# Kernel tuning notes

Measured on AMD Instinct MI355X. Metric: run time of the kernel, lower is better.

## Reference

```python
import jax, jax.numpy as jnp
import numpy as np

B, S, D = 2, 2048, 2048
H, DH = 16, 128
F = 5504
EPS = 1e-6
ROPE_THETA = 10000.0


def setup_inputs() -> dict:
    key = jax.random.key(0)
    ks = jax.random.split(key, 20)
    sc = 0.02
    r = lambda k, shape: (jax.random.normal(k, shape, dtype=jnp.float32) * sc)
    return {
        "hidden_states": jax.random.normal(ks[0], (B, S, D), dtype=jnp.float32),
        "ln1_w": jnp.ones((D,), jnp.float32),
        "wq": r(ks[1], (H * DH, D)), "bq": jnp.zeros((H * DH,), jnp.float32),
        "wk": r(ks[2], (H * DH, D)), "bk": jnp.zeros((H * DH,), jnp.float32),
        "wv": r(ks[3], (H * DH, D)), "bv": jnp.zeros((H * DH,), jnp.float32),
        "wo": r(ks[4], (D, H * DH)),
        "ln2_w": jnp.ones((D,), jnp.float32),
        "e1_gate": r(ks[5], (F, D)), "e1_up": r(ks[6], (F, D)), "e1_down": r(ks[7], (D, F)),
        "e2_gate": r(ks[8], (F, D)), "e2_up": r(ks[9], (F, D)), "e2_down": r(ks[10], (D, F)),
        "router_w": r(ks[11], (2, D)), "router_b": jnp.zeros((2,), jnp.float32),
    }


def rmsnorm(x, w):
    v = jnp.mean(x.astype(jnp.float32) ** 2, axis=-1, keepdims=True)
    return (x * jax.lax.rsqrt(v + EPS)).astype(x.dtype) * w


def rotate_half(x):
    x1, x2 = jnp.split(x, 2, axis=-1)
    return jnp.concatenate([-x2, x1], axis=-1)


def rope_cos_sin(seq_len, dtype):
    inv = 1.0 / (ROPE_THETA ** (jnp.arange(0, DH, 2, dtype=jnp.float32) / DH))
    t = jnp.arange(seq_len, dtype=jnp.float32)
    freqs = jnp.outer(t, inv)                      # [S, DH/2]
    emb = jnp.concatenate([freqs, freqs], axis=-1)  # [S, DH]
    return jnp.cos(emb).astype(dtype), jnp.sin(emb).astype(dtype)


def mlp(x, gate, up, down):
    return jnp.einsum('bsf,df->bsd', jax.nn.silu(jnp.einsum('bsd,fd->bsf', x, gate))
                      * jnp.einsum('bsd,fd->bsf', x, up), down)


def reference(hidden_states, ln1_w, wq, bq, wk, bk, wv, bv, wo, ln2_w,
              e1_gate, e1_up, e1_down, e2_gate, e2_up, e2_down,
              router_w, router_b):
    residual = hidden_states
    h = rmsnorm(hidden_states, ln1_w)

    # --- self attention with RoPE, causal ---
    q = (h @ wq.T + bq).reshape(B, S, H, DH).transpose(0, 2, 1, 3)  # [B,H,S,DH]
    k = (h @ wk.T + bk).reshape(B, S, H, DH).transpose(0, 2, 1, 3)
    v = (h @ wv.T + bv).reshape(B, S, H, DH).transpose(0, 2, 1, 3)
    cos, sin = rope_cos_sin(S, q.dtype)
    q = q * cos + rotate_half(q) * sin
    k = k * cos + rotate_half(k) * sin
    scores = jnp.einsum('bhqd,bhkd->bhqk', q, k) / jnp.sqrt(jnp.float32(DH))
    causal = jnp.tril(jnp.ones((S, S), dtype=bool))
    scores = jnp.where(causal, scores, jnp.finfo(scores.dtype).min)
    attn = jax.nn.softmax(scores, axis=-1)
    ctx = jnp.einsum('bhqk,bhkd->bhqd', attn, v).transpose(0, 2, 1, 3).reshape(B, S, H * DH)
    h = residual + ctx @ wo.T

    # --- MoE block: top-1 over 2 experts, both computed densely (as in source) ---
    residual = h
    h = rmsnorm(h, ln2_w)
    router_logits = h @ router_w.T + router_b          # [B,S,2]
    router_probs = jax.nn.softmax(router_logits, axis=-1)
    choice = jnp.argmax(router_probs, axis=-1)          # [B,S]
    m1 = (choice == 0).astype(h.dtype)[..., None]
    m2 = (choice == 1).astype(h.dtype)[..., None]
    out1 = mlp(h, e1_gate, e1_up, e1_down)
    out2 = mlp(h, e2_gate, e2_up, e2_down)
    return residual + m1 * out1 + m2 * out2
```

## Files before the change

kernel.cpp:

```cpp
#include <hip/hip_runtime.h>
#include <math.h>

typedef unsigned short u16;
typedef unsigned int u32;

#define D_ 2048
#define S_ 2048
#define DH_ 128
#define NH_ 16
#define F_ 5504
#define MTOK 4096

typedef __bf16 bf16x8 __attribute__((ext_vector_type(8)));
typedef float f32x4 __attribute__((ext_vector_type(4)));

__device__ __forceinline__ float bf2f(u32 u) {
  union { u32 i; float f; } x; x.i = u << 16; return x.f;
}
__device__ __forceinline__ u16 f2bf(float f) {
  u32 x = __float_as_uint(f);
  return (u16)((x + 0x7fffu + ((x >> 16) & 1u)) >> 16);
}

__global__ __launch_bounds__(256)
void k_f2bf(const float* __restrict__ src, u16* __restrict__ dst) {
  const size_t i = ((size_t)blockIdx.x * 256 + threadIdx.x) * 8;
  float4 a = *(const float4*)(src + i);
  float4 b = *(const float4*)(src + i + 4);
  uint4 p;
  p.x = f2bf(a.x) | ((u32)f2bf(a.y) << 16);
  p.y = f2bf(a.z) | ((u32)f2bf(a.w) << 16);
  p.z = f2bf(b.x) | ((u32)f2bf(b.y) << 16);
  p.w = f2bf(b.z) | ((u32)f2bf(b.w) << 16);
  *(uint4*)(dst + i) = p;
}

__global__ __launch_bounds__(256)
void k_moe_init(int* __restrict__ cnt, int* __restrict__ idx) {
  const int tid = threadIdx.x;
  if (tid < 2) cnt[tid] = 0;
  for (int i = tid; i < 2 * MTOK; i += 256) idx[i] = 0;
}

__global__ __launch_bounds__(256)
void k_rmsnorm1(const float* __restrict__ x, const float* __restrict__ w,
                u16* __restrict__ out) {
  const int t = blockIdx.x, tid = threadIdx.x;
  const size_t off = (size_t)t * D_ + tid * 8;
  float4 x0 = *(const float4*)(x + off);
  float4 x1 = *(const float4*)(x + off + 4);
  float v[8] = {x0.x, x0.y, x0.z, x0.w, x1.x, x1.y, x1.z, x1.w};
  float ss = 0.f;
  #pragma unroll
  for (int i = 0; i < 8; ++i) ss += v[i] * v[i];
  #pragma unroll
  for (int o = 32; o > 0; o >>= 1) ss += __shfl_xor(ss, o, 64);
  __shared__ float red[4];
  if ((tid & 63) == 0) red[tid >> 6] = ss;
  __syncthreads();
  const float tot = red[0] + red[1] + red[2] + red[3];
  const float rstd = 1.0f / sqrtf(tot / (float)D_ + 1e-6f);
  float4 w0 = *(const float4*)(w + tid * 8);
  float4 w1 = *(const float4*)(w + tid * 8 + 4);
  float wv[8] = {w0.x, w0.y, w0.z, w0.w, w1.x, w1.y, w1.z, w1.w};
  u32 hb[8];
  #pragma unroll
  for (int i = 0; i < 8; ++i) hb[i] = f2bf(v[i] * rstd * wv[i]);
  uint4 up;
  up.x = hb[0] | (hb[1] << 16); up.y = hb[2] | (hb[3] << 16);
  up.z = hb[4] | (hb[5] << 16); up.w = hb[6] | (hb[7] << 16);
  *(uint4*)(out + off) = up;
}

__global__ __launch_bounds__(256)
void k_rmsnorm2_router(const float* __restrict__ xin, const float* __restrict__ w,
                       const float* __restrict__ rw, const float* __restrict__ rb,
                       u16* __restrict__ h2, int* __restrict__ cnt,
                       int* __restrict__ idx) {
  const int t = blockIdx.x, tid = threadIdx.x;
  const size_t off = (size_t)t * D_ + tid * 8;
  float4 x0 = *(const float4*)(xin + off);
  float4 x1 = *(const float4*)(xin + off + 4);
  float v[8] = {x0.x, x0.y, x0.z, x0.w, x1.x, x1.y, x1.z, x1.w};
  float ss = 0.f;
  #pragma unroll
  for (int i = 0; i < 8; ++i) ss += v[i] * v[i];
  #pragma unroll
  for (int o = 32; o > 0; o >>= 1) ss += __shfl_xor(ss, o, 64);
  __shared__ float red[4];
  __shared__ float rl[8];
  if ((tid & 63) == 0) red[tid >> 6] = ss;
  __syncthreads();
  const float tot = red[0] + red[1] + red[2] + red[3];
  const float rstd = 1.0f / sqrtf(tot / (float)D_ + 1e-6f);
  float4 w0 = *(const float4*)(w + tid * 8);
  float4 w1 = *(const float4*)(w + tid * 8 + 4);
  float wv[8] = {w0.x, w0.y, w0.z, w0.w, w1.x, w1.y, w1.z, w1.w};
  float4 ra = *(const float4*)(rw + tid * 8);
  float4 rb4 = *(const float4*)(rw + tid * 8 + 4);
  float4 rc = *(const float4*)(rw + D_ + tid * 8);
  float4 rd = *(const float4*)(rw + D_ + tid * 8 + 4);
  float r0[8] = {ra.x, ra.y, ra.z, ra.w, rb4.x, rb4.y, rb4.z, rb4.w};
  float r1[8] = {rc.x, rc.y, rc.z, rc.w, rd.x, rd.y, rd.z, rd.w};
  float l0 = 0.f, l1 = 0.f;
  u32 hb[8];
  #pragma unroll
  for (int i = 0; i < 8; ++i) {
    const float h = v[i] * rstd * wv[i];
    hb[i] = f2bf(h);
    l0 += h * r0[i];
    l1 += h * r1[i];
  }
  uint4 up;
  up.x = hb[0] | (hb[1] << 16); up.y = hb[2] | (hb[3] << 16);
  up.z = hb[4] | (hb[5] << 16); up.w = hb[6] | (hb[7] << 16);
  *(uint4*)(h2 + off) = up;
  #pragma unroll
  for (int o = 32; o > 0; o >>= 1) {
    l0 += __shfl_xor(l0, o, 64);
    l1 += __shfl_xor(l1, o, 64);
  }
  if ((tid & 63) == 0) { rl[tid >> 6] = l0; rl[4 + (tid >> 6)] = l1; }
  __syncthreads();
  if (tid == 0) {
    const float L0 = rl[0] + rl[1] + rl[2] + rl[3] + rb[0];
    const float L1 = rl[4] + rl[5] + rl[6] + rl[7] + rb[1];
    const int e = (L1 > L0) ? 1 : 0;
    const int slot = atomicAdd(&cnt[e], 1);
    idx[e * MTOK + slot] = t;
  }
}

__global__ __launch_bounds__(256)
void k_rope_bf(const float* __restrict__ Q, const float* __restrict__ K,
               u16* __restrict__ Qo, u16* __restrict__ Ko) {
  const int t = blockIdx.x;
  const int s = t & (S_ - 1);
  const int d = threadIdx.x & 63;
  const int hq = threadIdx.x >> 6;
  const double inv = pow(10000.0, -(double)d / 64.0);
  const double ang = (double)s * inv;
  const float cf = (float)cos(ang);
  const float sf = (float)sin(ang);
  const float sc = 0.088388347648318447f;
  #pragma unroll
  for (int i = 0; i < 4; ++i) {
    const int h = hq * 4 + i;
    const size_t idx = (size_t)t * D_ + h * DH_ + d;
    float x1 = Q[idx], x2 = Q[idx + 64];
    Qo[idx]      = f2bf((x1 * cf - x2 * sf) * sc);
    Qo[idx + 64] = f2bf((x2 * cf + x1 * sf) * sc);
    float y1 = K[idx], y2 = K[idx + 64];
    Ko[idx]      = f2bf(y1 * cf - y2 * sf);
    Ko[idx + 64] = f2bf(y2 * cf + y1 * sf);
  }
}

__global__ __launch_bounds__(256)
void k_attn_mfma(const u16* __restrict__ Qbf, const u16* __restrict__ Kbf,
                 const u16* __restrict__ Vbf, u16* __restrict__ O) {
  __shared__ u16 Ks[64 * 128];
  __shared__ u16 Vt[128 * 64];
  __shared__ u16 Ps[4 * 16 * 64];
  const int qx = blockIdx.x, h = blockIdx.y, b = blockIdx.z;
  const int qt = (qx & 1) ? (31 - (qx >> 1)) : (qx >> 1);
  const int tid = threadIdx.x;
  const int w = tid >> 6, lane = tid & 63;
  const int quad = lane >> 4, l16 = lane & 15;

  const int q0 = qt * 64 + w * 16;
  const size_t qrow = (size_t)(b * S_ + q0 + l16) * D_ + h * DH_;
  bf16x8 qf[4];
  #pragma unroll
  for (int kd = 0; kd < 4; ++kd)
    qf[kd] = *(const bf16x8*)(Qbf + qrow + kd * 32 + quad * 8);

  f32x4 acc_o[8];
  #pragma unroll
  for (int i = 0; i < 8; ++i) acc_o[i] = 0;
  float mrun[4], lrun[4];
  #pragma unroll
  for (int r = 0; r < 4; ++r) { mrun[r] = -INFINITY; lrun[r] = 0.f; }

  const int nkt = qt + 1;
  const int vk = tid >> 2;
  const int vd0 = (tid & 3) * 32;

  for (int jt = 0; jt < nkt; ++jt) {
    const int kv0 = jt * 64;
    #pragma unroll
    for (int i = 0; i < 4; ++i) {
      const int slot = w * 256 + i * 64 + lane;
      const int r = slot >> 4, c = slot & 15;
      const int clog = (c & 8) | ((c & 7) ^ (r & 7));
      __builtin_amdgcn_global_load_lds(
        (const __attribute__((address_space(1))) void*)
          (Kbf + (size_t)(b * S_ + kv0 + r) * D_ + h * DH_ + clog * 8),
        (__attribute__((address_space(3))) void*)(Ks + (w * 256 + i * 64) * 8),
        16, 0, 0);
    }
    #pragma unroll
    for (int rr = 0; rr < 4; ++rr) {
      const int d0 = vd0 + rr * 8;
      bf16x8 vv = *(const bf16x8*)(Vbf + (size_t)(b * S_ + kv0 + vk) * D_ + h * DH_ + d0);
      const u16* pv = (const u16*)&vv;
      #pragma unroll
      for (int e = 0; e < 8; ++e) {
        const int d = d0 + e;
        Vt[d * 64 + ((((vk >> 3) ^ (d & 7) ^ ((d >> 5) & 3)) & 7) << 3) + (vk & 7)] = pv[e];
      }
    }
    __syncthreads();

    f32x4 st[4];
    #pragma unroll
    for (int nt = 0; nt < 4; ++nt) st[nt] = 0;
    #pragma unroll
    for (int kd = 0; kd < 4; ++kd) {
      #pragma unroll
      for (int nt = 0; nt < 4; ++nt) {
        const int kvr = nt * 16 + l16;
        const int c = kd * 4 + quad;
        const int p = (c & 8) | ((c & 7) ^ (kvr & 7));
        bf16x8 kf = *(const bf16x8*)(Ks + kvr * 128 + p * 8);
        st[nt] = __builtin_amdgcn_mfma_f32_16x16x32_bf16(qf[kd], kf, st[nt], 0, 0, 0);
      }
    }
    if (jt == qt) {
      #pragma unroll
      for (int nt = 0; nt < 4; ++nt) {
        const int kv = kv0 + nt * 16 + l16;
        #pragma unroll
        for (int r = 0; r < 4; ++r) {
          const int q = qt * 64 + w * 16 + quad * 4 + r;
          if (kv > q) st[nt][r] = -INFINITY;
        }
      }
    }
    float mx[4];
    #pragma unroll
    for (int r = 0; r < 4; ++r)
      mx[r] = fmaxf(fmaxf(st[0][r], st[1][r]), fmaxf(st[2][r], st[3][r]));
    #pragma unroll
    for (int o = 1; o < 16; o <<= 1) {
      #pragma unroll
      for (int r = 0; r < 4; ++r) mx[r] = fmaxf(mx[r], __shfl_xor(mx[r], o, 64));
    }
    float alpha[4], psum[4];
    #pragma unroll
    for (int r = 0; r < 4; ++r) {
      const float mnew = fmaxf(mrun[r], mx[r]);
      alpha[r] = expf(mrun[r] - mnew);
      mrun[r] = mnew;
      psum[r] = 0.f;
    }
    u16 pb[4][4];
    #pragma unroll
    for (int nt = 0; nt < 4; ++nt) {
      #pragma unroll
      for (int r = 0; r < 4; ++r) {
        const float p = expf(st[nt][r] - mrun[r]);
        psum[r] += p;
        pb[nt][r] = f2bf(p);
      }
    }
    #pragma unroll
    for (int o = 1; o < 16; o <<= 1) {
      #pragma unroll
      for (int r = 0; r < 4; ++r) psum[r] += __shfl_xor(psum[r], o, 64);
    }
    #pragma unroll
    for (int r = 0; r < 4; ++r) lrun[r] = lrun[r] * alpha[r] + psum[r];
    #pragma unroll
    for (int i = 0; i < 8; ++i) {
      #pragma unroll
      for (int r = 0; r < 4; ++r) acc_o[i][r] *= alpha[r];
    }
    const int wbase = w * 1024;
    #pragma unroll
    for (int nt = 0; nt < 4; ++nt) {
      #pragma unroll
      for (int r = 0; r < 4; ++r) {
        const int q = quad * 4 + r;
        const int cc = ((nt * 2 + (l16 >> 3)) ^ (q & 7) ^ (q >> 3)) & 7;
        Ps[wbase + q * 64 + cc * 8 + (l16 & 7)] = pb[nt][r];
      }
    }
    #pragma unroll
    for (int ks = 0; ks < 2; ++ks) {
      const int cP = ((ks * 4 + quad) ^ (l16 & 7) ^ (l16 >> 3)) & 7;
      bf16x8 pa = *(const bf16x8*)(Ps + wbase + l16 * 64 + cP * 8);
      #pragma unroll
      for (int nt = 0; nt < 8; ++nt) {
        const int d = nt * 16 + l16;
        const int cV = ((ks * 4 + quad) ^ (d & 7) ^ ((d >> 5) & 3)) & 7;
        bf16x8 vf = *(const bf16x8*)(Vt + d * 64 + cV * 8);
        acc_o[nt] = __builtin_amdgcn_mfma_f32_16x16x32_bf16(pa, vf, acc_o[nt], 0, 0, 0);
      }
    }
    __syncthreads();
  }
  float invl[4];
  #pragma unroll
  for (int r = 0; r < 4; ++r) invl[r] = 1.0f / lrun[r];
  #pragma unroll
  for (int r = 0; r < 4; ++r) {
    const size_t orow = (size_t)(b * S_ + qt * 64 + w * 16 + quad * 4 + r) * D_ + h * DH_;
    #pragma unroll
    for (int nt = 0; nt < 8; ++nt)
      O[orow + nt * 16 + l16] = f2bf(acc_o[nt][r] * invl[r]);
  }
}

template<int EPI>
__global__ __launch_bounds__(256)
void k_lin_bf16(const u16* __restrict__ A, const u16* __restrict__ W,
                const float* __restrict__ bias, const float* __restrict__ resf,
                void* Cv, int N, int K) {
  __shared__ u16 As[128 * 32];
  __shared__ u16 Bs[128 * 32];
  const int tid = threadIdx.x;
  const int wave = tid >> 6, lane = tid & 63;
  const int quad = lane >> 4, l16 = lane & 15;
  const int m0 = blockIdx.y * 128, n0 = blockIdx.x * 128;
  const int wm = (wave >> 1) * 64, wn = (wave & 1) * 64;
  f32x4 acc[4][4];
  #pragma unroll
  for (int i = 0; i < 4; ++i)
    #pragma unroll
    for (int j = 0; j < 4; ++j) acc[i][j] = 0;

  for (int k0 = 0; k0 < K; k0 += 32) {
    #pragma unroll
    for (int c = 0; c < 2; ++c) {
      const int ci = (c * 4 + wave) * 64 + lane;
      const int row = ci >> 2, ko = (ci & 3) << 3;
      __builtin_amdgcn_global_load_lds(
          (const __attribute__((address_space(1))) void*)(A + (size_t)(m0 + row) * K + k0 + ko),
          (__attribute__((address_space(3))) void*)(As + (size_t)(c * 4 + wave) * 512),
          16, 0, 0);
      __builtin_amdgcn_global_load_lds(
          (const __attribute__((address_space(1))) void*)(W + (size_t)(n0 + row) * K + k0 + ko),
          (__attribute__((address_space(3))) void*)(Bs + (size_t)(c * 4 + wave) * 512),
          16, 0, 0);
    }
    __syncthreads();
    bf16x8 af[4], bfr[4];
    #pragma unroll
    for (int i = 0; i < 4; ++i)
      af[i] = *(const bf16x8*)(As + (wm + i * 16 + l16) * 32 + quad * 8);
    #pragma unroll
    for (int j = 0; j < 4; ++j)
      bfr[j] = *(const bf16x8*)(Bs + (wn + j * 16 + l16) * 32 + quad * 8);
    #pragma unroll
    for (int i = 0; i < 4; ++i)
      #pragma unroll
      for (int j = 0; j < 4; ++j)
        acc[i][j] = __builtin_amdgcn_mfma_f32_16x16x32_bf16(af[i], bfr[j], acc[i][j], 0, 0, 0);
    __syncthreads();
  }

  #pragma unroll
  for (int i = 0; i < 4; ++i) {
    #pragma unroll
    for (int r = 0; r < 4; ++r) {
      const int row = m0 + wm + i * 16 + quad * 4 + r;
      #pragma unroll
      for (int j = 0; j < 4; ++j) {
        const int col = n0 + wn + j * 16 + l16;
        const float v = acc[i][j][r];
        const size_t idx = (size_t)row * N + col;
        if (EPI == 0) {
          ((float*)Cv)[idx] = v + bias[col];
        } else if (EPI == 1) {
          ((float*)Cv)[idx] = v + resf[idx];
        } else {
          ((u16*)Cv)[idx] = f2bf(v + bias[col]);
        }
      }
    }
  }
}

template<int EPI>
__global__ __launch_bounds__(256)
void k_moe_gup(const u16* __restrict__ A, const u16* __restrict__ W,
               const u16* __restrict__ gbuf, const int* __restrict__ idx,
               const int* __restrict__ cnt, u16* __restrict__ Cb, int N, int K) {
  const int m0 = blockIdx.y * 128;
  const int cn = *cnt;
  if (m0 >= cn) return;
  __shared__ u16 As[128 * 32];
  __shared__ u16 Bs[128 * 32];
  const int tid = threadIdx.x;
  const int wave = tid >> 6, lane = tid & 63;
  const int quad = lane >> 4, l16 = lane & 15;
  const int n0 = blockIdx.x * 128;
  const int wm = (wave >> 1) * 64, wn = (wave & 1) * 64;
  f32x4 acc[4][4];
  #pragma unroll
  for (int i = 0; i < 4; ++i)
    #pragma unroll
    for (int j = 0; j < 4; ++j) acc[i][j] = 0;

  int tokc[2], koc[2], wrow[2];
  #pragma unroll
  for (int c = 0; c < 2; ++c) {
    const int ci = (c * 4 + wave) * 64 + lane;
    const int row = ci >> 2;
    tokc[c] = idx[m0 + row];
    wrow[c] = row;
    koc[c] = (ci & 3) << 3;
  }

  for (int k0 = 0; k0 < K; k0 += 32) {
    #pragma unroll
    for (int c = 0; c < 2; ++c) {
      __builtin_amdgcn_global_load_lds(
          (const __attribute__((address_space(1))) void*)(A + (size_t)tokc[c] * K + k0 + koc[c]),
          (__attribute__((address_space(3))) void*)(As + (size_t)(c * 4 + wave) * 512),
          16, 0, 0);
      __builtin_amdgcn_global_load_lds(
          (const __attribute__((address_space(1))) void*)(W + (size_t)(n0 + wrow[c]) * K + k0 + koc[c]),
          (__attribute__((address_space(3))) void*)(Bs + (size_t)(c * 4 + wave) * 512),
          16, 0, 0);
    }
    __syncthreads();
    bf16x8 af[4], bfr[4];
    #pragma unroll
    for (int i = 0; i < 4; ++i)
      af[i] = *(const bf16x8*)(As + (wm + i * 16 + l16) * 32 + quad * 8);
    #pragma unroll
    for (int j = 0; j < 4; ++j)
      bfr[j] = *(const bf16x8*)(Bs + (wn + j * 16 + l16) * 32 + quad * 8);
    #pragma unroll
    for (int i = 0; i < 4; ++i)
      #pragma unroll
      for (int j = 0; j < 4; ++j)
        acc[i][j] = __builtin_amdgcn_mfma_f32_16x16x32_bf16(af[i], bfr[j], acc[i][j], 0, 0, 0);
    __syncthreads();
  }

  #pragma unroll
  for (int i = 0; i < 4; ++i) {
    #pragma unroll
    for (int r = 0; r < 4; ++r) {
      const int row = m0 + wm + i * 16 + quad * 4 + r;
      #pragma unroll
      for (int j = 0; j < 4; ++j) {
        const int col = n0 + wn + j * 16 + l16;
        const float v = acc[i][j][r];
        const size_t oidx = (size_t)row * N + col;
        if (EPI == 0) {
          Cb[oidx] = f2bf(v / (1.0f + expf(-v)));
        } else {
          Cb[oidx] = f2bf(v * bf2f(gbuf[oidx]));
        }
      }
    }
  }
}

__global__ __launch_bounds__(256)
void k_moe_down(const u16* __restrict__ A, const u16* __restrict__ W,
                const float* __restrict__ resf, const int* __restrict__ idx,
                const int* __restrict__ cnt, float* __restrict__ C, int N, int K) {
  const int m0 = blockIdx.y * 128;
  const int cn = *cnt;
  if (m0 >= cn) return;
  __shared__ u16 As[128 * 32];
  __shared__ u16 Bs[128 * 32];
  const int tid = threadIdx.x;
  const int wave = tid >> 6, lane = tid & 63;
  const int quad = lane >> 4, l16 = lane & 15;
  const int n0 = blockIdx.x * 128;
  const int wm = (wave >> 1) * 64, wn = (wave & 1) * 64;
  f32x4 acc[4][4];
  #pragma unroll
  for (int i = 0; i < 4; ++i)
    #pragma unroll
    for (int j = 0; j < 4; ++j) acc[i][j] = 0;

  for (int k0 = 0; k0 < K; k0 += 32) {
    #pragma unroll
    for (int c = 0; c < 2; ++c) {
      const int ci = (c * 4 + wave) * 64 + lane;
      const int row = ci >> 2, ko = (ci & 3) << 3;
      __builtin_amdgcn_global_load_lds(
          (const __attribute__((address_space(1))) void*)(A + (size_t)(m0 + row) * K + k0 + ko),
          (__attribute__((address_space(3))) void*)(As + (size_t)(c * 4 + wave) * 512),
          16, 0, 0);
      __builtin_amdgcn_global_load_lds(
          (const __attribute__((address_space(1))) void*)(W + (size_t)(n0 + row) * K + k0 + ko),
          (__attribute__((address_space(3))) void*)(Bs + (size_t)(c * 4 + wave) * 512),
          16, 0, 0);
    }
    __syncthreads();
    bf16x8 af[4], bfr[4];
    #pragma unroll
    for (int i = 0; i < 4; ++i)
      af[i] = *(const bf16x8*)(As + (wm + i * 16 + l16) * 32 + quad * 8);
    #pragma unroll
    for (int j = 0; j < 4; ++j)
      bfr[j] = *(const bf16x8*)(Bs + (wn + j * 16 + l16) * 32 + quad * 8);
    #pragma unroll
    for (int i = 0; i < 4; ++i)
      #pragma unroll
      for (int j = 0; j < 4; ++j)
        acc[i][j] = __builtin_amdgcn_mfma_f32_16x16x32_bf16(af[i], bfr[j], acc[i][j], 0, 0, 0);
    __syncthreads();
  }

  #pragma unroll
  for (int i = 0; i < 4; ++i) {
    #pragma unroll
    for (int r = 0; r < 4; ++r) {
      const int row = m0 + wm + i * 16 + quad * 4 + r;
      if (row < cn) {
        const int tok = idx[row];
        #pragma unroll
        for (int j = 0; j < 4; ++j) {
          const int col = n0 + wn + j * 16 + l16;
          const size_t oidx = (size_t)tok * N + col;
          C[oidx] = resf[oidx] + acc[i][j][r];
        }
      }
    }
  }
}

extern "C" void kernel_launch(void* const* d_in, const int* in_sizes, int n_in,
                              void* d_out, int out_size, void* d_ws, size_t ws_size,
                              hipStream_t stream) {
  (void)in_sizes; (void)n_in; (void)out_size; (void)ws_size;
  const float* hidden = (const float*)d_in[0];
  const float* ln1w   = (const float*)d_in[1];
  const float* wq     = (const float*)d_in[2];
  const float* bq     = (const float*)d_in[3];
  const float* wk     = (const float*)d_in[4];
  const float* bk     = (const float*)d_in[5];
  const float* wv     = (const float*)d_in[6];
  const float* bv     = (const float*)d_in[7];
  const float* wo     = (const float*)d_in[8];
  const float* ln2w   = (const float*)d_in[9];
  const float* e1g    = (const float*)d_in[10];
  const float* e1u    = (const float*)d_in[11];
  const float* e1d    = (const float*)d_in[12];
  const float* e2g    = (const float*)d_in[13];
  const float* e2u    = (const float*)d_in[14];
  const float* e2d    = (const float*)d_in[15];
  const float* rw     = (const float*)d_in[16];
  const float* rb     = (const float*)d_in[17];
  float* out = (float*)d_out;
  char* ws = (char*)d_ws;

  const size_t MB = 1024 * 1024;
  u16*   h1b  = (u16*)(ws);
  float* Qb   = (float*)(ws + 16 * MB);
  float* Kb   = (float*)(ws + 48 * MB);
  u16*   Qbf  = (u16*)(ws + 80 * MB);
  u16*   Kbf  = (u16*)(ws + 96 * MB);
  u16*   Vbf  = (u16*)(ws + 112 * MB);
  u16*   ctxb = (u16*)(ws + 128 * MB);
  float* res2 = Qb;
  u16*   h2b  = (u16*)(ws + 48 * MB);
  int*   idx  = (int*)(ws + 128 * MB);
  int*   cnt  = (int*)(ws + 128 * MB + 64 * 1024);
  u16*   act  = (u16*)(ws + 80 * MB);
  u16*   wlin = (u16*)(ws + 144 * MB);
  u16*   wbf  = (u16*)(ws + 144 * MB);

  k_rmsnorm1<<<MTOK, 256, 0, stream>>>(hidden, ln1w, h1b);

  const int WD = (D_ * D_) / 8 / 256;
  const int WCONV = (F_ * D_) / 8 / 256;
  dim3 gQKV(D_ / 128, MTOK / 128);

  k_f2bf<<<WD, 256, 0, stream>>>(wq, wlin);
  k_lin_bf16<0><<<gQKV, 256, 0, stream>>>(h1b, wlin, bq, nullptr, Qb, D_, D_);
  k_f2bf<<<WD, 256, 0, stream>>>(wk, wlin);
  k_lin_bf16<0><<<gQKV, 256, 0, stream>>>(h1b, wlin, bk, nullptr, Kb, D_, D_);
  k_f2bf<<<WD, 256, 0, stream>>>(wv, wlin);
  k_lin_bf16<2><<<gQKV, 256, 0, stream>>>(h1b, wlin, bv, nullptr, Vbf, D_, D_);

  k_rope_bf<<<MTOK, 256, 0, stream>>>(Qb, Kb, Qbf, Kbf);
  k_attn_mfma<<<dim3(32, NH_, 2), 256, 0, stream>>>(Qbf, Kbf, Vbf, ctxb);

  k_f2bf<<<WD, 256, 0, stream>>>(wo, wlin);
  k_lin_bf16<1><<<gQKV, 256, 0, stream>>>(ctxb, wlin, nullptr, hidden, res2, D_, D_);

  k_moe_init<<<1, 256, 0, stream>>>(cnt, idx);
  k_rmsnorm2_router<<<MTOK, 256, 0, stream>>>(res2, ln2w, rw, rb, h2b, cnt, idx);

  dim3 gFU(F_ / 128, MTOK / 128), gDN(D_ / 128, MTOK / 128);

  k_f2bf<<<WCONV, 256, 0, stream>>>(e1g, wbf);
  k_moe_gup<0><<<gFU, 256, 0, stream>>>(h2b, wbf, nullptr, idx, cnt, act, F_, D_);
  k_f2bf<<<WCONV, 256, 0, stream>>>(e1u, wbf);
  k_moe_gup<1><<<gFU, 256, 0, stream>>>(h2b, wbf, act, idx, cnt, act, F_, D_);
  k_f2bf<<<WCONV, 256, 0, stream>>>(e1d, wbf);
  k_moe_down<<<gDN, 256, 0, stream>>>(act, wbf, res2, idx, cnt, out, D_, F_);
  k_f2bf<<<WCONV, 256, 0, stream>>>(e2g, wbf);
  k_moe_gup<0><<<gFU, 256, 0, stream>>>(h2b, wbf, nullptr, idx + MTOK, cnt + 1, act, F_, D_);
  k_f2bf<<<WCONV, 256, 0, stream>>>(e2u, wbf);
  k_moe_gup<1><<<gFU, 256, 0, stream>>>(h2b, wbf, act, idx + MTOK, cnt + 1, act, F_, D_);
  k_f2bf<<<WCONV, 256, 0, stream>>>(e2d, wbf);
  k_moe_down<<<gDN, 256, 0, stream>>>(act, wbf, res2, idx + MTOK, cnt + 1, out, D_, F_);
}
```

Before: 1.680 ms.

## Write V transposed from projection epilogue and async-load it in attention

```diff
diff --git a/kernel.cpp b/kernel.cpp
--- a/kernel.cpp
+++ b/kernel.cpp
@@ -158,9 +158,9 @@
 
 __global__ __launch_bounds__(256)
 void k_attn_mfma(const u16* __restrict__ Qbf, const u16* __restrict__ Kbf,
-                 const u16* __restrict__ Vbf, u16* __restrict__ O) {
+                 const u16* __restrict__ VT, u16* __restrict__ O) {
   __shared__ u16 Ks[64 * 128];
-  __shared__ u16 Vt[128 * 64];
+  __shared__ u16 Vs[128 * 64];
   __shared__ u16 Ps[4 * 16 * 64];
   const int qx = blockIdx.x, h = blockIdx.y, b = blockIdx.z;
   const int qt = (qx & 1) ? (31 - (qx >> 1)) : (qx >> 1);
@@ -182,39 +182,42 @@
   #pragma unroll
   for (int r = 0; r < 4; ++r) { mrun[r] = -INFINITY; lrun[r] = 0.f; }
 
+  const u16* vtbase = VT + (size_t)(b * NH_ + h) * DH_ * S_;
+  const u16* kbase  = Kbf + (size_t)(b) * S_ * D_ + h * DH_;
+  int krow[4], kcol[4], vrow[4], vcol[4];
+  #pragma unroll
+  for (int i = 0; i < 4; ++i) {
+    const int slot = w * 256 + i * 64 + lane;
+    const int kr = slot >> 4, kc = slot & 15;
+    krow[i] = kr;
+    kcol[i] = ((kc & 8) | ((kc & 7) ^ (kr & 7))) * 8;
+    const int vr = slot >> 3, vc = slot & 7;
+    vrow[i] = vr;
+    vcol[i] = (vc ^ (vr & 7)) * 8;
+  }
+
   const int nkt = qt + 1;
-  const int vk = tid >> 2;
-  const int vd0 = (tid & 3) * 32;
-
   for (int jt = 0; jt < nkt; ++jt) {
     const int kv0 = jt * 64;
     #pragma unroll
     for (int i = 0; i < 4; ++i) {
-      const int slot = w * 256 + i * 64 + lane;
-      const int r = slot >> 4, c = slot & 15;
-      const int clog = (c & 8) | ((c & 7) ^ (r & 7));
       __builtin_amdgcn_global_load_lds(
         (const __attribute__((address_space(1))) void*)
-          (Kbf + (size_t)(b * S_ + kv0 + r) * D_ + h * DH_ + clog * 8),
+          (kbase + (size_t)(kv0 + krow[i]) * D_ + kcol[i]),
         (__attribute__((address_space(3))) void*)(Ks + (w * 256 + i * 64) * 8),
         16, 0, 0);
-    }
-    #pragma unroll
-    for (int rr = 0; rr < 4; ++rr) {
-      const int d0 = vd0 + rr * 8;
-      bf16x8 vv = *(const bf16x8*)(Vbf + (size_t)(b * S_ + kv0 + vk) * D_ + h * DH_ + d0);
-      const u16* pv = (const u16*)&vv;
-      #pragma unroll
-      for (int e = 0; e < 8; ++e) {
-        const int d = d0 + e;
-        Vt[d * 64 + ((((vk >> 3) ^ (d & 7) ^ ((d >> 5) & 3)) & 7) << 3) + (vk & 7)] = pv[e];
-      }
+      __builtin_amdgcn_global_load_lds(
+        (const __attribute__((address_space(1))) void*)
+          (vtbase + (size_t)vrow[i] * S_ + kv0 + vcol[i]),
+        (__attribute__((address_space(3))) void*)(Vs + (w * 256 + i * 64) * 8),
+        16, 0, 0);
     }
     __syncthreads();
 
     f32x4 st[4];
     #pragma unroll
     for (int nt = 0; nt < 4; ++nt) st[nt] = 0;
+    __builtin_amdgcn_s_setprio(1);
     #pragma unroll
     for (int kd = 0; kd < 4; ++kd) {
       #pragma unroll
@@ -226,6 +229,7 @@
         st[nt] = __builtin_amdgcn_mfma_f32_16x16x32_bf16(qf[kd], kf, st[nt], 0, 0, 0);
       }
     }
+    __builtin_amdgcn_s_setprio(0);
     if (jt == qt) {
       #pragma unroll
       for (int nt = 0; nt < 4; ++nt) {
@@ -286,6 +290,7 @@
         Ps[wbase + q * 64 + cc * 8 + (l16 & 7)] = pb[nt][r];
       }
     }
+    __builtin_amdgcn_s_setprio(1);
     #pragma unroll
     for (int ks = 0; ks < 2; ++ks) {
       const int cP = ((ks * 4 + quad) ^ (l16 & 7) ^ (l16 >> 3)) & 7;
@@ -293,11 +298,12 @@
       #pragma unroll
       for (int nt = 0; nt < 8; ++nt) {
         const int d = nt * 16 + l16;
-        const int cV = ((ks * 4 + quad) ^ (d & 7) ^ ((d >> 5) & 3)) & 7;
-        bf16x8 vf = *(const bf16x8*)(Vt + d * 64 + cV * 8);
+        const int cV = ((ks * 4 + quad) ^ (d & 7)) & 7;
+        bf16x8 vf = *(const bf16x8*)(Vs + d * 64 + cV * 8);
         acc_o[nt] = __builtin_amdgcn_mfma_f32_16x16x32_bf16(pa, vf, acc_o[nt], 0, 0, 0);
       }
     }
+    __builtin_amdgcn_s_setprio(0);
     __syncthreads();
   }
   float invl[4];
@@ -360,6 +366,28 @@
     __syncthreads();
   }
 
+  if (EPI == 3) {
+    u16* vt = (u16*)Cv;
+    #pragma unroll
+    for (int i = 0; i < 4; ++i) {
+      const int row0 = m0 + wm + i * 16 + quad * 4;
+      const int bb = row0 >> 11, s0 = row0 & (S_ - 1);
+      #pragma unroll
+      for (int j = 0; j < 4; ++j) {
+        const int col = n0 + wn + j * 16 + l16;
+        const float bv = bias[col];
+        ushort4 p;
+        p.x = f2bf(acc[i][j][0] + bv);
+        p.y = f2bf(acc[i][j][1] + bv);
+        p.z = f2bf(acc[i][j][2] + bv);
+        p.w = f2bf(acc[i][j][3] + bv);
+        const size_t vtr = (size_t)((bb * NH_ + (col >> 7)) * DH_ + (col & (DH_ - 1)));
+        *(ushort4*)(vt + vtr * S_ + s0) = p;
+      }
+    }
+    return;
+  }
+
   #pragma unroll
   for (int i = 0; i < 4; ++i) {
     #pragma unroll
@@ -374,8 +402,6 @@
           ((float*)Cv)[idx] = v + bias[col];
         } else if (EPI == 1) {
           ((float*)Cv)[idx] = v + resf[idx];
-        } else {
-          ((u16*)Cv)[idx] = f2bf(v + bias[col]);
         }
       }
     }
@@ -560,7 +586,7 @@
   float* Kb   = (float*)(ws + 48 * MB);
   u16*   Qbf  = (u16*)(ws + 80 * MB);
   u16*   Kbf  = (u16*)(ws + 96 * MB);
-  u16*   Vbf  = (u16*)(ws + 112 * MB);
+  u16*   VT   = (u16*)(ws + 112 * MB);
   u16*   ctxb = (u16*)(ws + 128 * MB);
   float* res2 = Qb;
   u16*   h2b  = (u16*)(ws + 48 * MB);
@@ -581,10 +607,10 @@
   k_f2bf<<<WD, 256, 0, stream>>>(wk, wlin);
   k_lin_bf16<0><<<gQKV, 256, 0, stream>>>(h1b, wlin, bk, nullptr, Kb, D_, D_);
   k_f2bf<<<WD, 256, 0, stream>>>(wv, wlin);
-  k_lin_bf16<2><<<gQKV, 256, 0, stream>>>(h1b, wlin, bv, nullptr, Vbf, D_, D_);
+  k_lin_bf16<3><<<gQKV, 256, 0, stream>>>(h1b, wlin, bv, nullptr, VT, D_, D_);
 
   k_rope_bf<<<MTOK, 256, 0, stream>>>(Qb, Kb, Qbf, Kbf);
-  k_attn_mfma<<<dim3(32, NH_, 2), 256, 0, stream>>>(Qbf, Kbf, Vbf, ctxb);
+  k_attn_mfma<<<dim3(32, NH_, 2), 256, 0, stream>>>(Qbf, Kbf, VT, ctxb);
 
   k_f2bf<<<WD, 256, 0, stream>>>(wo, wlin);
   k_lin_bf16<1><<<gQKV, 256, 0, stream>>>(ctxb, wlin, nullptr, hidden, res2, D_, D_);
```

Result: faster. 1.568 ms (-6.7%).
